# Optimization experiments

Hardware: AMD Instinct MI355X
Metric: run time of the kernel (lower is better)

Reference implementation:

```python
import jax, jax.numpy as jnp
import numpy as np

N = 50000        # nodes
E = 400000       # edges
F_IN = 128       # node feature dim
NEG_SLOPE = 0.2  # PyG GATConv default


def setup_inputs() -> dict:
    key = jax.random.key(0)
    ks = jax.random.split(key, 24)
    p = lambda k, shape: (jax.random.normal(k, shape, dtype=jnp.float32) * 0.1)
    return {
        "x": jax.random.normal(ks[0], (N, F_IN), dtype=jnp.float32),
        "edge_index": jax.random.randint(ks[1], (2, E), 0, N, dtype=jnp.int32),
        "edge_attr": jax.random.normal(ks[2], (E, 1), dtype=jnp.float32),
        "year": jax.random.normal(ks[3], (E, 1), dtype=jnp.float32),
        "quarter": jax.random.normal(ks[4], (E, 1), dtype=jnp.float32),
        "W1": p(ks[5], (4 * 128, F_IN)), "a1s": p(ks[6], (4, 128)), "a1d": p(ks[7], (4, 128)), "b1": jnp.zeros((512,), jnp.float32),
        "W2": p(ks[8], (4 * 32, 512)), "a2s": p(ks[9], (4, 32)), "a2d": p(ks[10], (4, 32)), "b2": jnp.zeros((128,), jnp.float32),
        "W3": p(ks[11], (1 * 8, 128)), "a3s": p(ks[12], (1, 8)), "a3d": p(ks[13], (1, 8)), "b3": jnp.zeros((8,), jnp.float32),
        # fc1: 8*2 + 1 + 2 = 19 -> 16 ; fc2: 16 -> 1
        "fc1_w": p(ks[14], (16, 19)), "fc1_b": jnp.zeros((16,), jnp.float32),
        "fc2_w": p(ks[15], (1, 16)), "fc2_b": jnp.zeros((1,), jnp.float32),
    }


def gat_conv(x, src, dst, W, a_s, a_d, b):
    """PyG GATConv (concat=True, self-loops already in src/dst, no dropout)."""
    H, C = a_s.shape
    n = x.shape[0]
    h = (x @ W.T).reshape(n, H, C)                      # [N,H,C]
    s = jnp.einsum("nhc,hc->nh", h, a_s)                # alpha_src per node
    d = jnp.einsum("nhc,hc->nh", h, a_d)                # alpha_dst per node
    e = jax.nn.leaky_relu(s[src] + d[dst], NEG_SLOPE)   # [E',H]
    m = jax.ops.segment_max(e, dst, num_segments=n)     # segment softmax over dst
    ex = jnp.exp(e - m[dst])
    den = jax.ops.segment_sum(ex, dst, num_segments=n)
    alpha = ex / den[dst]                               # [E',H]
    out = jax.ops.segment_sum(alpha[:, :, None] * h[src], dst, num_segments=n)
    return out.reshape(n, H * C) + b


def reference(x, edge_index, edge_attr, year, quarter,
              W1, a1s, a1d, b1, W2, a2s, a2d, b2, W3, a3s, a3d, b3,
              fc1_w, fc1_b, fc2_w, fc2_b):
    n = x.shape[0]
    loops = jnp.arange(n, dtype=edge_index.dtype)       # add_self_loops=True
    src = jnp.concatenate([edge_index[0], loops])
    dst = jnp.concatenate([edge_index[1], loops])
    h = jax.nn.elu(gat_conv(x, src, dst, W1, a1s, a1d, b1))
    h = jax.nn.elu(gat_conv(h, src, dst, W2, a2s, a2d, b2))
    h = jax.nn.elu(gat_conv(h, src, dst, W3, a3s, a3d, b3))
    z = jnp.concatenate([h[edge_index[0]], h[edge_index[1]], edge_attr, year, quarter], axis=1)
    z = jax.nn.relu(z @ fc1_w.T + fc1_b)
    return (z @ fc2_w.T + fc2_b).squeeze(-1)            # [E]
```

## Files before the change

kernel.cpp:

```cpp
#include <hip/hip_runtime.h>
#include <hip/hip_bf16.h>

#define NN 50000
#define EE 400000
#define EP 450000

typedef __attribute__((ext_vector_type(8))) short short8;
typedef __attribute__((ext_vector_type(4))) float f32x4;

__device__ __forceinline__ float us2f(unsigned short u) {
    unsigned int x = ((unsigned int)u) << 16;
    union { unsigned int i; float f; } c; c.i = x; return c.f;
}
__device__ __forceinline__ unsigned short f2bfu(float f) {
    union { float f; unsigned int u; } c; c.f = f;
    unsigned int r = c.u + 0x7FFFu + ((c.u >> 16) & 1u);
    return (unsigned short)(r >> 16);
}
__device__ __forceinline__ unsigned int pack2bf(float lo, float hi) {
    return (unsigned int)f2bfu(lo) | ((unsigned int)f2bfu(hi) << 16);
}
__device__ __forceinline__ float lrelu_exp(float x) {
    x = x > 0.f ? x : 0.2f * x;
    return __expf(x);
}


#define DEGB 1758
#define CVTB 512
__global__ void prep_kernel(const int* __restrict__ ei, int* __restrict__ deg,
                            const float* __restrict__ W1, const float* __restrict__ W2,
                            __hip_bfloat16* __restrict__ pw1, __hip_bfloat16* __restrict__ pw2,
                            const float* __restrict__ a1s, const float* __restrict__ a1d,
                            float* __restrict__ usd) {
    int b = blockIdx.x;
    if (b < DEGB) {
        int e = b * 256 + threadIdx.x;
        if (e >= EP) return;
        int dst = (e < EE) ? ei[EE + e] : e - EE;
        atomicAdd(&deg[dst], 1);
    } else if (b < DEGB + CVTB) {
        int i = (b - DEGB) * 256 + threadIdx.x;
        if (i < 65536) {
            int n = i >> 7, k = i & 127;
            int idx = ((n >> 4) * 4 + (k >> 5)) * 512 + ((k & 31) >> 3) * 128 + (n & 15) * 8 + (k & 7);
            pw1[idx] = __float2bfloat16(W1[i]);
        } else {
            int j = i - 65536;
            int n = j >> 9, k = j & 511;
            int idx = ((n >> 4) * 16 + (k >> 5)) * 512 + ((k & 31) >> 3) * 128 + (n & 15) * 8 + (k & 7);
            pw2[idx] = __float2bfloat16(W2[j]);
        }
    } else {
        int t = (b - DEGB - CVTB) * 256 + threadIdx.x;
        if (t >= 1024) return;
        int row = t >> 7, k = t & 127;
        int hh = row & 3;
        const float* av = (row < 4) ? (a1s + hh * 128) : (a1d + hh * 128);
        const float* wp = W1 + (size_t)(hh * 128) * 128 + k;
        float acc = 0.f;
        for (int c = 0; c < 128; c++) acc += av[c] * wp[(size_t)c * 128];
        usd[t] = acc;
    }
}

__global__ void cvtx_sd(const float* __restrict__ x, const float* __restrict__ usd,
                        __hip_bfloat16* __restrict__ xb,
                        float* __restrict__ s, float* __restrict__ d, int M) {
    __shared__ float us_s[1024];
    for (int i = threadIdx.x; i < 1024; i += 256) us_s[i] = usd[i];
    __syncthreads();
    int wave = threadIdx.x >> 6, lane = threadIdx.x & 63;
    int m0 = blockIdx.x * 64 + wave * 16;
    int r = lane & 15, quad = lane >> 4;
    int am = m0 + r; if (am >= M) am = M - 1;
    const float* xp = x + (size_t)am * 128 + quad * 8;
    float xv[32];
#pragma unroll
    for (int kk = 0; kk < 4; kk++) {
        float4 a = *(const float4*)(xp + kk * 32);
        float4 bq = *(const float4*)(xp + kk * 32 + 4);
        xv[kk*8+0]=a.x;  xv[kk*8+1]=a.y;  xv[kk*8+2]=a.z;  xv[kk*8+3]=a.w;
        xv[kk*8+4]=bq.x; xv[kk*8+5]=bq.y; xv[kk*8+6]=bq.z; xv[kk*8+7]=bq.w;
        short8 o;
        o[0]=(short)f2bfu(a.x);  o[1]=(short)f2bfu(a.y);
        o[2]=(short)f2bfu(a.z);  o[3]=(short)f2bfu(a.w);
        o[4]=(short)f2bfu(bq.x); o[5]=(short)f2bfu(bq.y);
        o[6]=(short)f2bfu(bq.z); o[7]=(short)f2bfu(bq.w);
        *(short8*)(xb + (size_t)am * 128 + quad * 8 + kk * 32) = o;
    }
    float acc[8];
#pragma unroll
    for (int o = 0; o < 8; o++) {
        const float* up = us_s + o * 128 + quad * 8;
        float a = 0.f;
#pragma unroll
        for (int kk = 0; kk < 4; kk++)
#pragma unroll
            for (int j = 0; j < 8; j++) a += xv[kk*8+j] * up[kk*32+j];
        acc[o] = a;
    }
#pragma unroll
    for (int o = 0; o < 8; o++) {
        acc[o] += __shfl_xor(acc[o], 16, 64);
        acc[o] += __shfl_xor(acc[o], 32, 64);
    }
    int m = m0 + r;
    if (quad == 0 && m < M) {
#pragma unroll
        for (int hh = 0; hh < 4; hh++) { s[m*4+hh] = acc[hh]; d[m*4+hh] = acc[4+hh]; }
    }
}

#define SCB 49
__global__ void scan1_kernel(const int* __restrict__ deg, int* __restrict__ bsum) {
    __shared__ int red[256];
    int b = blockIdx.x, t = threadIdx.x;
    int base = b * 1024 + t * 4;
    int s = 0;
    if (base + 3 < NN) { int4 v = *(const int4*)(deg + base); s = v.x + v.y + v.z + v.w; }
    else { for (int i = base; i < NN; i++) s += deg[i]; }
    red[t] = s;
    __syncthreads();
    for (int off = 128; off > 0; off >>= 1) {
        if (t < off) red[t] += red[t + off];
        __syncthreads();
    }
    if (t == 0) bsum[b] = red[0];
}

__global__ void scan2_kernel(const int* __restrict__ deg, const int* __restrict__ bsum,
                             int* __restrict__ offsets) {
    __shared__ int lsum[256];
    int b = blockIdx.x, t = threadIdx.x;
    int boff = 0;
    for (int i = 0; i < b; i++) boff += bsum[i];
    int base = b * 1024 + t * 4;
    int4 v = {0, 0, 0, 0};
    if (base + 3 < NN) v = *(const int4*)(deg + base);
    else {
        if (base < NN)     v.x = deg[base];
        if (base + 1 < NN) v.y = deg[base + 1];
        if (base + 2 < NN) v.z = deg[base + 2];
        if (base + 3 < NN) v.w = deg[base + 3];
    }
    int s = v.x + v.y + v.z + v.w;
    lsum[t] = s;
    __syncthreads();
    for (int off = 1; off < 256; off <<= 1) {
        int val = (t >= off) ? lsum[t - off] : 0;
        __syncthreads();
        lsum[t] += val;
        __syncthreads();
    }
    int ex = boff + (t ? lsum[t - 1] : 0);
    if (base < NN)     offsets[base]     = ex;
    if (base + 1 < NN) offsets[base + 1] = ex + v.x;
    if (base + 2 < NN) offsets[base + 2] = ex + v.x + v.y;
    if (base + 3 < NN) offsets[base + 3] = ex + v.x + v.y + v.z;
    if (b == SCB - 1 && t == 255) offsets[NN] = boff + lsum[255];
}

__global__ void fill_kernel(const int* __restrict__ ei, const int* __restrict__ offsets,
                            int* __restrict__ cursor,
                            const float* __restrict__ s1, const float* __restrict__ d1,
                            int* __restrict__ elist, int* __restrict__ dstlist,
                            float* __restrict__ welist) {
    int e = blockIdx.x * blockDim.x + threadIdx.x;
    if (e >= EP) return;
    int src, dst;
    if (e < EE) { src = ei[e]; dst = ei[EE + e]; } else { src = dst = e - EE; }
    int pos = atomicAdd(&cursor[dst], 1);
    int j = offsets[dst] + pos;
    elist[j] = src;
    dstlist[j] = dst;
    float4 sv = *(const float4*)(s1 + (size_t)src * 4);
    float4 dv = *(const float4*)(d1 + (size_t)dst * 4);
    float4 w;
    w.x = lrelu_exp(sv.x + dv.x);
    w.y = lrelu_exp(sv.y + dv.y);
    w.z = lrelu_exp(sv.z + dv.z);
    w.w = lrelu_exp(sv.w + dv.w);
    *(float4*)(welist + (size_t)j * 4) = w;
}

__global__ void edge_w4(const int* __restrict__ elist, const int* __restrict__ dstlist,
                        const float* __restrict__ s, const float* __restrict__ d,
                        float* __restrict__ wout) {
    int j = blockIdx.x * blockDim.x + threadIdx.x;
    if (j >= EP) return;
    int src = elist[j], dst = dstlist[j];
    float4 sv = *(const float4*)(s + (size_t)src * 4);
    float4 dv = *(const float4*)(d + (size_t)dst * 4);
    float4 w;
    w.x = lrelu_exp(sv.x + dv.x);
    w.y = lrelu_exp(sv.y + dv.y);
    w.z = lrelu_exp(sv.z + dv.z);
    w.w = lrelu_exp(sv.w + dv.w);
    *(float4*)(wout + (size_t)j * 4) = w;
}

__global__ void edge_w1(const int* __restrict__ elist, const int* __restrict__ dstlist,
                        const float* __restrict__ s, const float* __restrict__ d,
                        float* __restrict__ wout) {
    int j = blockIdx.x * blockDim.x + threadIdx.x;
    if (j >= EP) return;
    wout[j] = lrelu_exp(s[elist[j]] + d[dstlist[j]]);
}

__global__ __launch_bounds__(1024) void l1_fused(
        const int* __restrict__ elist, const int* __restrict__ offsets,
        const float* __restrict__ wl,
        const __hip_bfloat16* __restrict__ xb,
        const __hip_bfloat16* __restrict__ pW1,
        const float* __restrict__ b,
        __hip_bfloat16* __restrict__ pact) {
    __shared__ unsigned short frag[16 * 520];
    int w = threadIdx.x >> 6, lane = threadIdx.x & 63;
    int m0 = blockIdx.x * 16;
    int node = m0 + w;

    int j0 = __builtin_amdgcn_readfirstlane(offsets[node]);
    int j1 = __builtin_amdgcn_readfirstlane(offsets[node + 1]);
    float den0 = 0.f, den1 = 0.f, den2 = 0.f, den3 = 0.f;
    float a00=0.f,a01=0.f,a10=0.f,a11=0.f,a20=0.f,a21=0.f,a30=0.f,a31=0.f;
    const unsigned short* xp = (const unsigned short*)xb + lane * 2;
    int j = j0;
    for (; j + 4 <= j1; j += 4) {
        int sA = elist[j], sB = elist[j+1], sC = elist[j+2], sD = elist[j+3];
        float4 wA = *(const float4*)(wl + (size_t)j * 4);
        float4 wB = *(const float4*)(wl + (size_t)(j+1) * 4);
        float4 wC = *(const float4*)(wl + (size_t)(j+2) * 4);
        float4 wD = *(const float4*)(wl + (size_t)(j+3) * 4);
        unsigned int xA = *(const unsigned int*)(xp + (size_t)sA * 128);
        unsigned int xB = *(const unsigned int*)(xp + (size_t)sB * 128);
        unsigned int xC = *(const unsigned int*)(xp + (size_t)sC * 128);
        unsigned int xD = *(const unsigned int*)(xp + (size_t)sD * 128);
        float xA0 = us2f((unsigned short)xA), xA1 = us2f((unsigned short)(xA >> 16));
        float xB0 = us2f((unsigned short)xB), xB1 = us2f((unsigned short)(xB >> 16));
        float xC0 = us2f((unsigned short)xC), xC1 = us2f((unsigned short)(xC >> 16));
        float xD0 = us2f((unsigned short)xD), xD1 = us2f((unsigned short)(xD >> 16));
        den0 += (wA.x + wB.x) + (wC.x + wD.x);
        den1 += (wA.y + wB.y) + (wC.y + wD.y);
        den2 += (wA.z + wB.z) + (wC.z + wD.z);
        den3 += (wA.w + wB.w) + (wC.w + wD.w);
        a00 += wA.x*xA0 + wB.x*xB0 + wC.x*xC0 + wD.x*xD0;
        a01 += wA.x*xA1 + wB.x*xB1 + wC.x*xC1 + wD.x*xD1;
        a10 += wA.y*xA0 + wB.y*xB0 + wC.y*xC0 + wD.y*xD0;
        a11 += wA.y*xA1 + wB.y*xB1 + wC.y*xC1 + wD.y*xD1;
        a20 += wA.z*xA0 + wB.z*xB0 + wC.z*xC0 + wD.z*xD0;
        a21 += wA.z*xA1 + wB.z*xB1 + wC.z*xC1 + wD.z*xD1;
        a30 += wA.w*xA0 + wB.w*xB0 + wC.w*xC0 + wD.w*xD0;
        a31 += wA.w*xA1 + wB.w*xB1 + wC.w*xC1 + wD.w*xD1;
    }
    for (; j < j1; j++) {
        int sE = elist[j];
        float4 ww = *(const float4*)(wl + (size_t)j * 4);
        unsigned int xv = *(const unsigned int*)(xp + (size_t)sE * 128);
        float x0 = us2f((unsigned short)xv), x1 = us2f((unsigned short)(xv >> 16));
        den0 += ww.x; den1 += ww.y; den2 += ww.z; den3 += ww.w;
        a00 += ww.x*x0; a01 += ww.x*x1; a10 += ww.y*x0; a11 += ww.y*x1;
        a20 += ww.z*x0; a21 += ww.z*x1; a30 += ww.w*x0; a31 += ww.w*x1;
    }
    {
        int c0 = lane * 2;
        int fq = c0 >> 5;
        int sub = (c0 & 31) >> 3;
        int rowp = w ^ (sub << 2);
        float i0 = 1.f/den0, i1 = 1.f/den1, i2 = 1.f/den2, i3 = 1.f/den3;
        unsigned int* f32p = (unsigned int*)frag;
        int base = (fq * 520 + sub * 128 + rowp * 8 + (c0 & 7)) >> 1;
        f32p[base]             = pack2bf(a00*i0, a01*i0);
        f32p[base + 4 * 260]   = pack2bf(a10*i1, a11*i1);
        f32p[base + 8 * 260]   = pack2bf(a20*i2, a21*i2);
        f32p[base + 12 * 260]  = pack2bf(a30*i3, a31*i3);
    }
    __syncthreads();

    int hh = w >> 2, g = w & 3;
    int r = lane & 15, quad = lane >> 4;
    int lsub = lane >> 4, lrow = lane & 15;
    int prow = lrow ^ (lsub << 2);
    const unsigned short* fb = frag + lsub * 128 + prow * 8;
    short8 afrag[4];
#pragma unroll
    for (int kk = 0; kk < 4; kk++)
        afrag[kk] = *(const short8*)(fb + (hh * 4 + kk) * 520);
#pragma unroll
    for (int t = 0; t < 2; t++) {
        int nb = g * 32 + t * 16;
        const __hip_bfloat16* bp = pW1 + ((size_t)(hh * 8 + (nb >> 4)) * 4) * 512 + lane * 8;
        f32x4 acc = {0.f, 0.f, 0.f, 0.f};
#pragma unroll
        for (int kk = 0; kk < 4; kk++) {
            short8 bfr = *(const short8*)(bp + kk * 512);
            acc = __builtin_amdgcn_mfma_f32_16x16x32_bf16(afrag[kk], bfr, acc, 0, 0, 0);
        }
        int n0 = hh * 128 + nb;
        float bias = b[n0 + r];
        int kk2 = (n0 + r) >> 5;
        int sub2 = ((nb & 16) + r) >> 3;
        __hip_bfloat16* op = pact + ((size_t)blockIdx.x * 16 + kk2) * 512
                           + sub2 * 128 + (r & 7);
#pragma unroll
        for (int i = 0; i < 4; i++) {
            float v = acc[i] + bias;
            v = v > 0.f ? v : (__expf(v) - 1.0f);
            op[(quad * 4 + i) * 8] = __float2bfloat16(v);
        }
    }
}

__global__ void gemm_l2(const __hip_bfloat16* __restrict__ pA,
                        const __hip_bfloat16* __restrict__ pW2,
                        const float* __restrict__ as_, const float* __restrict__ ad_,
                        __hip_bfloat16* __restrict__ Cb,
                        float* __restrict__ s, float* __restrict__ d, int M) {
    int hh = threadIdx.x >> 6, lane = threadIdx.x & 63;
    int m0 = blockIdx.x * 16;
    int r = lane & 15, quad = lane >> 4;
    const __hip_bfloat16* ap  = pA + (size_t)(m0 >> 4) * 16 * 512 + lane * 8;
    const __hip_bfloat16* bp0 = pW2 + (size_t)(hh * 2) * 16 * 512 + lane * 8;
    const __hip_bfloat16* bp1 = bp0 + 16 * 512;
    f32x4 acc0 = {0.f, 0.f, 0.f, 0.f}, acc1 = {0.f, 0.f, 0.f, 0.f};
#pragma unroll
    for (int kk = 0; kk < 16; kk++) {
        short8 af = *(const short8*)(ap + kk * 512);
        short8 b0 = *(const short8*)(bp0 + kk * 512);
        short8 b1 = *(const short8*)(bp1 + kk * 512);
        acc0 = __builtin_amdgcn_mfma_f32_16x16x32_bf16(af, b0, acc0, 0, 0, 0);
        acc1 = __builtin_amdgcn_mfma_f32_16x16x32_bf16(af, b1, acc1, 0, 0, 0);
    }
    int n0 = hh * 32;
    float as0 = as_[n0 + r],      ad0 = ad_[n0 + r];
    float as1 = as_[n0 + 16 + r], ad1 = ad_[n0 + 16 + r];
    float sacc[4], dacc[4];
#pragma unroll
    for (int i = 0; i < 4; i++) {
        int m = m0 + quad * 4 + i;
        Cb[(size_t)m * 128 + n0 + r]      = __float2bfloat16(acc0[i]);
        Cb[(size_t)m * 128 + n0 + 16 + r] = __float2bfloat16(acc1[i]);
        sacc[i] = acc0[i] * as0 + acc1[i] * as1;
        dacc[i] = acc0[i] * ad0 + acc1[i] * ad1;
    }
#pragma unroll
    for (int mask = 1; mask <= 8; mask <<= 1) {
#pragma unroll
        for (int i = 0; i < 4; i++) {
            sacc[i] += __shfl_xor(sacc[i], mask, 64);
            dacc[i] += __shfl_xor(dacc[i], mask, 64);
        }
    }
    if (r == 0) {
#pragma unroll
        for (int i = 0; i < 4; i++) {
            int m = m0 + quad * 4 + i;
            s[m * 4 + hh] = sacc[i]; d[m * 4 + hh] = dacc[i];
        }
    }
}

__global__ void gather_l2_g8(const int* __restrict__ elist, const int* __restrict__ offsets,
                             const float* __restrict__ wl,
                             const __hip_bfloat16* __restrict__ h,
                             const float* __restrict__ b,
                             const float* __restrict__ W3,
                             const float* __restrict__ a3s, const float* __restrict__ a3d,
                             __hip_bfloat16* __restrict__ h3,
                             float* __restrict__ s, float* __restrict__ d) {
    int gid = blockIdx.x * blockDim.x + threadIdx.x;
    if (gid >= NN * 64) return;
    int node = gid >> 6;
    int lane = gid & 63;
    int c0 = lane * 2;
    int hh = lane >> 4;
    int j0 = __builtin_amdgcn_readfirstlane(offsets[node]);
    int j1 = __builtin_amdgcn_readfirstlane(offsets[node + 1]);
    float den = 0.f, acc0 = 0.f, acc1 = 0.f;
    const unsigned short* hp = (const unsigned short*)h + c0;
    int j = j0;
    for (; j + 4 <= j1; j += 4) {
        int sA = elist[j], sB = elist[j+1], sC = elist[j+2], sD = elist[j+3];
        float wA = wl[(size_t)j*4 + hh],     wB = wl[(size_t)(j+1)*4 + hh];
        float wC = wl[(size_t)(j+2)*4 + hh], wD = wl[(size_t)(j+3)*4 + hh];
        unsigned int vA = *(const unsigned int*)(hp + (size_t)sA * 128);
        unsigned int vB = *(const unsigned int*)(hp + (size_t)sB * 128);
        unsigned int vC = *(const unsigned int*)(hp + (size_t)sC * 128);
        unsigned int vD = *(const unsigned int*)(hp + (size_t)sD * 128);
        den += (wA + wB) + (wC + wD);
        acc0 += wA * us2f((unsigned short)vA) + wB * us2f((unsigned short)vB)
              + wC * us2f((unsigned short)vC) + wD * us2f((unsigned short)vD);
        acc1 += wA * us2f((unsigned short)(vA >> 16)) + wB * us2f((unsigned short)(vB >> 16))
              + wC * us2f((unsigned short)(vC >> 16)) + wD * us2f((unsigned short)(vD >> 16));
    }
    for (; j < j1; j++) {
        int sE = elist[j];
        float ww = wl[(size_t)j*4 + hh];
        unsigned int v = *(const unsigned int*)(hp + (size_t)sE * 128);
        den += ww;
        acc0 += ww * us2f((unsigned short)v);
        acc1 += ww * us2f((unsigned short)(v >> 16));
    }
    float inv = 1.0f / den;
    float v0 = acc0 * inv + b[c0];
    float v1 = acc1 * inv + b[c0 + 1];
    v0 = v0 > 0.f ? v0 : (__expf(v0) - 1.0f);
    v1 = v1 > 0.f ? v1 : (__expf(v1) - 1.0f);
    float part[8];
#pragma unroll
    for (int c = 0; c < 8; c++) {
        float2 wv = *(const float2*)(W3 + c * 128 + c0);
        part[c] = v0 * wv.x + v1 * wv.y;
    }
#pragma unroll
    for (int mask = 1; mask < 64; mask <<= 1) {
#pragma unroll
        for (int c = 0; c < 8; c++) part[c] += __shfl_xor(part[c], mask, 64);
    }
    if (lane < 8) h3[(size_t)node * 8 + lane] = __float2bfloat16(part[lane]);
    if (lane == 0) {
        float sv = 0.f, dv = 0.f;
#pragma unroll
        for (int c = 0; c < 8; c++) { sv += part[c] * a3s[c]; dv += part[c] * a3d[c]; }
        s[node] = sv; d[node] = dv;
    }
}

__global__ void gather_l3(const int* __restrict__ elist, const int* __restrict__ offsets,
                          const float* __restrict__ wl,
                          const __hip_bfloat16* __restrict__ h,
                          const float* __restrict__ b,
                          __hip_bfloat16* __restrict__ act) {
    int gid = blockIdx.x * blockDim.x + threadIdx.x;
    if (gid >= NN * 8) return;
    int node = gid >> 3, t = gid & 7;
    int j0 = offsets[node], j1 = offsets[node + 1];
    float den = 0.f, acc = 0.f;
    const unsigned short* hp = (const unsigned short*)h + t;
    int j = j0;
    for (; j + 4 <= j1; j += 4) {
        int sA = elist[j], sB = elist[j+1], sC = elist[j+2], sD = elist[j+3];
        float wA = wl[j], wB = wl[j+1], wC = wl[j+2], wD = wl[j+3];
        float xA = us2f(hp[(size_t)sA * 8]);
        float xB = us2f(hp[(size_t)sB * 8]);
        float xC = us2f(hp[(size_t)sC * 8]);
        float xD = us2f(hp[(size_t)sD * 8]);
        den += (wA + wB) + (wC + wD);
        acc += wA * xA + wB * xB + wC * xC + wD * xD;
    }
    for (; j < j1; j++) {
        int sE = elist[j];
        float w = wl[j];
        den += w;
        acc += w * us2f(hp[(size_t)sE * 8]);
    }
    float v = acc / den + b[t];
    v = v > 0.f ? v : (__expf(v) - 1.0f);
    act[(size_t)node * 8 + t] = __float2bfloat16(v);
}

__global__ void mlp_kernel(const int* __restrict__ ei,
                           const __hip_bfloat16* __restrict__ act3,
                           const float* __restrict__ ea,
                           const float* __restrict__ yr,
                           const float* __restrict__ qt,
                           const float* __restrict__ fc1w,
                           const float* __restrict__ fc1b,
                           const float* __restrict__ fc2w,
                           const float* __restrict__ fc2b,
                           float* __restrict__ outp) {
    __shared__ float w1[16 * 19], b1s[16], w2[16];
    for (int i = threadIdx.x; i < 16 * 19; i += blockDim.x) w1[i] = fc1w[i];
    if (threadIdx.x < 16) {
        b1s[threadIdx.x] = fc1b[threadIdx.x];
        w2[threadIdx.x] = fc2w[threadIdx.x];
    }
    __syncthreads();
    int e = blockIdx.x * blockDim.x + threadIdx.x;
    if (e >= EE) return;
    int src = ei[e], dst = ei[EE + e];
    short8 hs = *(const short8*)(act3 + (size_t)src * 8);
    short8 hd = *(const short8*)(act3 + (size_t)dst * 8);
    float z[19];
#pragma unroll
    for (int i = 0; i < 8; i++) z[i] = us2f((unsigned short)hs[i]);
#pragma unroll
    for (int i = 0; i < 8; i++) z[8 + i] = us2f((unsigned short)hd[i]);
    z[16] = ea[e]; z[17] = yr[e]; z[18] = qt[e];
    float acc2 = fc2b[0];
#pragma unroll
    for (int j = 0; j < 16; j++) {
        float a = b1s[j];
#pragma unroll
        for (int i = 0; i < 19; i++) a += z[i] * w1[j * 19 + i];
        a = a > 0.f ? a : 0.f;
        acc2 += a * w2[j];
    }
    outp[e] = acc2;
}

extern "C" void kernel_launch(void* const* d_in, const int* in_sizes, int n_in,
                              void* d_out, int out_size, void* d_ws, size_t ws_size,
                              hipStream_t stream) {
    const float* x    = (const float*)d_in[0];
    const int*   ei   = (const int*)d_in[1];
    const float* ea   = (const float*)d_in[2];
    const float* yr   = (const float*)d_in[3];
    const float* qt   = (const float*)d_in[4];
    const float* W1   = (const float*)d_in[5];
    const float* a1s  = (const float*)d_in[6];
    const float* a1d  = (const float*)d_in[7];
    const float* b1   = (const float*)d_in[8];
    const float* W2   = (const float*)d_in[9];
    const float* a2s  = (const float*)d_in[10];
    const float* a2d  = (const float*)d_in[11];
    const float* b2   = (const float*)d_in[12];
    const float* W3   = (const float*)d_in[13];
    const float* a3s  = (const float*)d_in[14];
    const float* a3d  = (const float*)d_in[15];
    const float* b3   = (const float*)d_in[16];
    const float* fc1w = (const float*)d_in[17];
    const float* fc1b = (const float*)d_in[18];
    const float* fc2w = (const float*)d_in[19];
    const float* fc2b = (const float*)d_in[20];
    float* outp = (float*)d_out;

    char* ws = (char*)d_ws;
    __hip_bfloat16* h_buf   = (__hip_bfloat16*)(ws);
    __hip_bfloat16* act_buf = (__hip_bfloat16*)(ws + 51200000);
    float* s_buf   = (float*)(ws + 102400000);
    float* d_buf   = (float*)(ws + 103200000);
    int*   deg     = (int*)  (ws + 104000000);
    int*   cursor  = (int*)  (ws + 104200000);
    int*   offsets = (int*)  (ws + 104400000);
    int*   elist   = (int*)  (ws + 104600016);
    __hip_bfloat16* pw1 = (__hip_bfloat16*)(ws + 106400016);
    __hip_bfloat16* pw2 = (__hip_bfloat16*)(ws + 106531088);
    float* usd  = (float*)(ws + 106662160);
    int*   bsum = (int*)  (ws + 106666256);
    float* welist = (float*)(ws + 106666512);
    int*   dstlist = (int*)(ws + 113866512);
    __hip_bfloat16* xb = act_buf;

    hipMemsetAsync(deg, 0, 2 * NN * sizeof(int), stream);
    prep_kernel<<<DEGB + CVTB + 4, 256, 0, stream>>>(ei, deg, W1, W2, pw1, pw2, a1s, a1d, usd);
    scan1_kernel<<<SCB, 256, 0, stream>>>(deg, bsum);
    scan2_kernel<<<SCB, 256, 0, stream>>>(deg, bsum, offsets);
    cvtx_sd<<<(NN + 63) / 64, 256, 0, stream>>>(x, usd, xb, s_buf, d_buf, NN);
    fill_kernel<<<(EP + 255) / 256, 256, 0, stream>>>(ei, offsets, cursor, s_buf, d_buf,
                                                      elist, dstlist, welist);

    l1_fused<<<NN / 16, 1024, 0, stream>>>(elist, offsets, welist, xb, pw1, b1, h_buf);

    gemm_l2<<<(NN + 15) / 16, 256, 0, stream>>>(
        h_buf, pw2, a2s, a2d, act_buf, s_buf, d_buf, NN);
    edge_w4<<<(EP + 255) / 256, 256, 0, stream>>>(elist, dstlist, s_buf, d_buf, welist);

    gather_l2_g8<<<(NN * 64 + 255) / 256, 256, 0, stream>>>(
        elist, offsets, welist, act_buf, b2, W3, a3s, a3d, h_buf, s_buf, d_buf);

    edge_w1<<<(EP + 255) / 256, 256, 0, stream>>>(elist, dstlist, s_buf, d_buf, welist);
    gather_l3<<<(NN * 8 + 255) / 256, 256, 0, stream>>>(
        elist, offsets, welist, h_buf, b3, act_buf);

    mlp_kernel<<<(EE + 255) / 256, 256, 0, stream>>>(ei, act_buf, ea, yr, qt,
                                                     fc1w, fc1b, fc2w, fc2b, outp);
}
```

Baseline: 308.4 us.

## Fuse edge-weight computation into gathers and process two nodes per wave in layer 1

Removes the edge_w4 and edge_w1 kernels and the dstlist buffer. Layers 2 and 3 now compute the leaky-relu and exp attention weights inline in the gather loops from per-node s/d scores, with separate s3/d3 buffers so layer-3 scores no longer overwrite the layer-2 ones being read. This saves two launches and the edge-weight write/read traffic, at the cost of redundant exp work per lane and an extra random gather of s2. The layer-1 fused kernel drops to 512 threads, each wave aggregating two destination nodes with interleaved loops and four MFMA column tiles instead of two.

```diff
diff --git a/kernel.cpp b/kernel.cpp
--- a/kernel.cpp
+++ b/kernel.cpp
@@ -164,8 +164,7 @@
 __global__ void fill_kernel(const int* __restrict__ ei, const int* __restrict__ offsets,
                             int* __restrict__ cursor,
                             const float* __restrict__ s1, const float* __restrict__ d1,
-                            int* __restrict__ elist, int* __restrict__ dstlist,
-                            float* __restrict__ welist) {
+                            int* __restrict__ elist, float* __restrict__ welist) {
     int e = blockIdx.x * blockDim.x + threadIdx.x;
     if (e >= EP) return;
     int src, dst;
@@ -173,7 +172,6 @@
     int pos = atomicAdd(&cursor[dst], 1);
     int j = offsets[dst] + pos;
     elist[j] = src;
-    dstlist[j] = dst;
     float4 sv = *(const float4*)(s1 + (size_t)src * 4);
     float4 dv = *(const float4*)(d1 + (size_t)dst * 4);
     float4 w;
@@ -184,31 +182,17 @@
     *(float4*)(welist + (size_t)j * 4) = w;
 }
 
-__global__ void edge_w4(const int* __restrict__ elist, const int* __restrict__ dstlist,
-                        const float* __restrict__ s, const float* __restrict__ d,
-                        float* __restrict__ wout) {
-    int j = blockIdx.x * blockDim.x + threadIdx.x;
-    if (j >= EP) return;
-    int src = elist[j], dst = dstlist[j];
-    float4 sv = *(const float4*)(s + (size_t)src * 4);
-    float4 dv = *(const float4*)(d + (size_t)dst * 4);
-    float4 w;
-    w.x = lrelu_exp(sv.x + dv.x);
-    w.y = lrelu_exp(sv.y + dv.y);
-    w.z = lrelu_exp(sv.z + dv.z);
-    w.w = lrelu_exp(sv.w + dv.w);
-    *(float4*)(wout + (size_t)j * 4) = w;
-}
-
-__global__ void edge_w1(const int* __restrict__ elist, const int* __restrict__ dstlist,
-                        const float* __restrict__ s, const float* __restrict__ d,
-                        float* __restrict__ wout) {
-    int j = blockIdx.x * blockDim.x + threadIdx.x;
-    if (j >= EP) return;
-    wout[j] = lrelu_exp(s[elist[j]] + d[dstlist[j]]);
-}
-
-__global__ __launch_bounds__(1024) void l1_fused(
+__device__ __forceinline__ void acc_edge(float (&den)[4], float (&acc)[8],
+                                         float4 w, unsigned int x) {
+    float x0 = us2f((unsigned short)x), x1 = us2f((unsigned short)(x >> 16));
+    den[0] += w.x; den[1] += w.y; den[2] += w.z; den[3] += w.w;
+    acc[0] += w.x * x0; acc[1] += w.x * x1;
+    acc[2] += w.y * x0; acc[3] += w.y * x1;
+    acc[4] += w.z * x0; acc[5] += w.z * x1;
+    acc[6] += w.w * x0; acc[7] += w.w * x1;
+}
+
+__global__ void l1_fused(
         const int* __restrict__ elist, const int* __restrict__ offsets,
         const float* __restrict__ wl,
         const __hip_bfloat16* __restrict__ xb,
@@ -218,66 +202,87 @@
     __shared__ unsigned short frag[16 * 520];
     int w = threadIdx.x >> 6, lane = threadIdx.x & 63;
     int m0 = blockIdx.x * 16;
-    int node = m0 + w;
-
-    int j0 = __builtin_amdgcn_readfirstlane(offsets[node]);
-    int j1 = __builtin_amdgcn_readfirstlane(offsets[node + 1]);
-    float den0 = 0.f, den1 = 0.f, den2 = 0.f, den3 = 0.f;
-    float a00=0.f,a01=0.f,a10=0.f,a11=0.f,a20=0.f,a21=0.f,a30=0.f,a31=0.f;
+    int nA = m0 + 2 * w;
+
+    int ja  = __builtin_amdgcn_readfirstlane(offsets[nA]);
+    int jA1 = __builtin_amdgcn_readfirstlane(offsets[nA + 1]);
+    int jB1 = __builtin_amdgcn_readfirstlane(offsets[nA + 2]);
+    int jb = jA1;
+
+    float dA[4] = {0.f,0.f,0.f,0.f}, dB[4] = {0.f,0.f,0.f,0.f};
+    float aA[8] = {0.f,0.f,0.f,0.f,0.f,0.f,0.f,0.f};
+    float aB[8] = {0.f,0.f,0.f,0.f,0.f,0.f,0.f,0.f};
     const unsigned short* xp = (const unsigned short*)xb + lane * 2;
-    int j = j0;
-    for (; j + 4 <= j1; j += 4) {
-        int sA = elist[j], sB = elist[j+1], sC = elist[j+2], sD = elist[j+3];
-        float4 wA = *(const float4*)(wl + (size_t)j * 4);
-        float4 wB = *(const float4*)(wl + (size_t)(j+1) * 4);
-        float4 wC = *(const float4*)(wl + (size_t)(j+2) * 4);
-        float4 wD = *(const float4*)(wl + (size_t)(j+3) * 4);
-        unsigned int xA = *(const unsigned int*)(xp + (size_t)sA * 128);
-        unsigned int xB = *(const unsigned int*)(xp + (size_t)sB * 128);
-        unsigned int xC = *(const unsigned int*)(xp + (size_t)sC * 128);
-        unsigned int xD = *(const unsigned int*)(xp + (size_t)sD * 128);
-        float xA0 = us2f((unsigned short)xA), xA1 = us2f((unsigned short)(xA >> 16));
-        float xB0 = us2f((unsigned short)xB), xB1 = us2f((unsigned short)(xB >> 16));
-        float xC0 = us2f((unsigned short)xC), xC1 = us2f((unsigned short)(xC >> 16));
-        float xD0 = us2f((unsigned short)xD), xD1 = us2f((unsigned short)(xD >> 16));
-        den0 += (wA.x + wB.x) + (wC.x + wD.x);
-        den1 += (wA.y + wB.y) + (wC.y + wD.y);
-        den2 += (wA.z + wB.z) + (wC.z + wD.z);
-        den3 += (wA.w + wB.w) + (wC.w + wD.w);
-        a00 += wA.x*xA0 + wB.x*xB0 + wC.x*xC0 + wD.x*xD0;
-        a01 += wA.x*xA1 + wB.x*xB1 + wC.x*xC1 + wD.x*xD1;
-        a10 += wA.y*xA0 + wB.y*xB0 + wC.y*xC0 + wD.y*xD0;
-        a11 += wA.y*xA1 + wB.y*xB1 + wC.y*xC1 + wD.y*xD1;
-        a20 += wA.z*xA0 + wB.z*xB0 + wC.z*xC0 + wD.z*xD0;
-        a21 += wA.z*xA1 + wB.z*xB1 + wC.z*xC1 + wD.z*xD1;
-        a30 += wA.w*xA0 + wB.w*xB0 + wC.w*xC0 + wD.w*xD0;
-        a31 += wA.w*xA1 + wB.w*xB1 + wC.w*xC1 + wD.w*xD1;
-    }
-    for (; j < j1; j++) {
-        int sE = elist[j];
-        float4 ww = *(const float4*)(wl + (size_t)j * 4);
-        unsigned int xv = *(const unsigned int*)(xp + (size_t)sE * 128);
-        float x0 = us2f((unsigned short)xv), x1 = us2f((unsigned short)(xv >> 16));
-        den0 += ww.x; den1 += ww.y; den2 += ww.z; den3 += ww.w;
-        a00 += ww.x*x0; a01 += ww.x*x1; a10 += ww.y*x0; a11 += ww.y*x1;
-        a20 += ww.z*x0; a21 += ww.z*x1; a30 += ww.w*x0; a31 += ww.w*x1;
-    }
+    const float4* wl4 = (const float4*)wl;
+
+    while (ja + 2 <= jA1 && jb + 2 <= jB1) {
+        int s0 = elist[ja], s1 = elist[ja + 1];
+        int s2 = elist[jb], s3 = elist[jb + 1];
+        float4 w0 = wl4[ja], w1 = wl4[ja + 1];
+        float4 w2 = wl4[jb], w3 = wl4[jb + 1];
+        unsigned int x0 = *(const unsigned int*)(xp + (size_t)s0 * 128);
+        unsigned int x1 = *(const unsigned int*)(xp + (size_t)s1 * 128);
+        unsigned int x2 = *(const unsigned int*)(xp + (size_t)s2 * 128);
+        unsigned int x3 = *(const unsigned int*)(xp + (size_t)s3 * 128);
+        acc_edge(dA, aA, w0, x0); acc_edge(dA, aA, w1, x1);
+        acc_edge(dB, aB, w2, x2); acc_edge(dB, aB, w3, x3);
+        ja += 2; jb += 2;
+    }
+    while (ja + 2 <= jA1) {
+        int s0 = elist[ja], s1 = elist[ja + 1];
+        float4 w0 = wl4[ja], w1 = wl4[ja + 1];
+        unsigned int x0 = *(const unsigned int*)(xp + (size_t)s0 * 128);
+        unsigned int x1 = *(const unsigned int*)(xp + (size_t)s1 * 128);
+        acc_edge(dA, aA, w0, x0); acc_edge(dA, aA, w1, x1);
+        ja += 2;
+    }
+    while (jb + 2 <= jB1) {
+        int s0 = elist[jb], s1 = elist[jb + 1];
+        float4 w0 = wl4[jb], w1 = wl4[jb + 1];
+        unsigned int x0 = *(const unsigned int*)(xp + (size_t)s0 * 128);
+        unsigned int x1 = *(const unsigned int*)(xp + (size_t)s1 * 128);
+        acc_edge(dB, aB, w0, x0); acc_edge(dB, aB, w1, x1);
+        jb += 2;
+    }
+    if (ja < jA1) {
+        int s0 = elist[ja]; float4 w0 = wl4[ja];
+        unsigned int x0 = *(const unsigned int*)(xp + (size_t)s0 * 128);
+        acc_edge(dA, aA, w0, x0);
+    }
+    if (jb < jB1) {
+        int s0 = elist[jb]; float4 w0 = wl4[jb];
+        unsigned int x0 = *(const unsigned int*)(xp + (size_t)s0 * 128);
+        acc_edge(dB, aB, w0, x0);
+    }
+
     {
         int c0 = lane * 2;
         int fq = c0 >> 5;
         int sub = (c0 & 31) >> 3;
-        int rowp = w ^ (sub << 2);
-        float i0 = 1.f/den0, i1 = 1.f/den1, i2 = 1.f/den2, i3 = 1.f/den3;
         unsigned int* f32p = (unsigned int*)frag;
-        int base = (fq * 520 + sub * 128 + rowp * 8 + (c0 & 7)) >> 1;
-        f32p[base]             = pack2bf(a00*i0, a01*i0);
-        f32p[base + 4 * 260]   = pack2bf(a10*i1, a11*i1);
-        f32p[base + 8 * 260]   = pack2bf(a20*i2, a21*i2);
-        f32p[base + 12 * 260]  = pack2bf(a30*i3, a31*i3);
+        int base0 = fq * 260 + sub * 64 + (c0 & 7) / 2;
+        {
+            int rowp = (2 * w) ^ (sub << 2);
+            int base = base0 + rowp * 4;
+            float i0 = 1.f/dA[0], i1 = 1.f/dA[1], i2 = 1.f/dA[2], i3 = 1.f/dA[3];
+            f32p[base]            = pack2bf(aA[0]*i0, aA[1]*i0);
+            f32p[base + 4 * 260]  = pack2bf(aA[2]*i1, aA[3]*i1);
+            f32p[base + 8 * 260]  = pack2bf(aA[4]*i2, aA[5]*i2);
+            f32p[base + 12 * 260] = pack2bf(aA[6]*i3, aA[7]*i3);
+        }
+        {
+            int rowp = (2 * w + 1) ^ (sub << 2);
+            int base = base0 + rowp * 4;
+            float i0 = 1.f/dB[0], i1 = 1.f/dB[1], i2 = 1.f/dB[2], i3 = 1.f/dB[3];
+            f32p[base]            = pack2bf(aB[0]*i0, aB[1]*i0);
+            f32p[base + 4 * 260]  = pack2bf(aB[2]*i1, aB[3]*i1);
+            f32p[base + 8 * 260]  = pack2bf(aB[4]*i2, aB[5]*i2);
+            f32p[base + 12 * 260] = pack2bf(aB[6]*i3, aB[7]*i3);
+        }
     }
     __syncthreads();
 
-    int hh = w >> 2, g = w & 3;
+    int hh = w >> 1, half = w & 1;
     int r = lane & 15, quad = lane >> 4;
     int lsub = lane >> 4, lrow = lane & 15;
     int prow = lrow ^ (lsub << 2);
@@ -287,8 +292,8 @@
     for (int kk = 0; kk < 4; kk++)
         afrag[kk] = *(const short8*)(fb + (hh * 4 + kk) * 520);
 #pragma unroll
-    for (int t = 0; t < 2; t++) {
-        int nb = g * 32 + t * 16;
+    for (int t = 0; t < 4; t++) {
+        int nb = half * 64 + t * 16;
         const __hip_bfloat16* bp = pW1 + ((size_t)(hh * 8 + (nb >> 4)) * 4) * 512 + lane * 8;
         f32x4 acc = {0.f, 0.f, 0.f, 0.f};
 #pragma unroll
@@ -361,13 +366,13 @@
 }
 
 __global__ void gather_l2_g8(const int* __restrict__ elist, const int* __restrict__ offsets,
-                             const float* __restrict__ wl,
+                             const float* __restrict__ s2, const float* __restrict__ d2,
                              const __hip_bfloat16* __restrict__ h,
                              const float* __restrict__ b,
                              const float* __restrict__ W3,
                              const float* __restrict__ a3s, const float* __restrict__ a3d,
                              __hip_bfloat16* __restrict__ h3,
-                             float* __restrict__ s, float* __restrict__ d) {
+                             float* __restrict__ s3, float* __restrict__ d3) {
     int gid = blockIdx.x * blockDim.x + threadIdx.x;
     if (gid >= NN * 64) return;
     int node = gid >> 6;
@@ -376,17 +381,20 @@
     int hh = lane >> 4;
     int j0 = __builtin_amdgcn_readfirstlane(offsets[node]);
     int j1 = __builtin_amdgcn_readfirstlane(offsets[node + 1]);
+    float dv = d2[node * 4 + hh];
     float den = 0.f, acc0 = 0.f, acc1 = 0.f;
     const unsigned short* hp = (const unsigned short*)h + c0;
     int j = j0;
     for (; j + 4 <= j1; j += 4) {
         int sA = elist[j], sB = elist[j+1], sC = elist[j+2], sD = elist[j+3];
-        float wA = wl[(size_t)j*4 + hh],     wB = wl[(size_t)(j+1)*4 + hh];
-        float wC = wl[(size_t)(j+2)*4 + hh], wD = wl[(size_t)(j+3)*4 + hh];
+        float eA = s2[sA * 4 + hh] + dv, eB = s2[sB * 4 + hh] + dv;
+        float eC = s2[sC * 4 + hh] + dv, eD = s2[sD * 4 + hh] + dv;
         unsigned int vA = *(const unsigned int*)(hp + (size_t)sA * 128);
         unsigned int vB = *(const unsigned int*)(hp + (size_t)sB * 128);
         unsigned int vC = *(const unsigned int*)(hp + (size_t)sC * 128);
         unsigned int vD = *(const unsigned int*)(hp + (size_t)sD * 128);
+        float wA = lrelu_exp(eA), wB = lrelu_exp(eB);
+        float wC = lrelu_exp(eC), wD = lrelu_exp(eD);
         den += (wA + wB) + (wC + wD);
         acc0 += wA * us2f((unsigned short)vA) + wB * us2f((unsigned short)vB)
               + wC * us2f((unsigned short)vC) + wD * us2f((unsigned short)vD);
@@ -395,7 +403,7 @@
     }
     for (; j < j1; j++) {
         int sE = elist[j];
-        float ww = wl[(size_t)j*4 + hh];
+        float ww = lrelu_exp(s2[sE * 4 + hh] + dv);
         unsigned int v = *(const unsigned int*)(hp + (size_t)sE * 128);
         den += ww;
         acc0 += ww * us2f((unsigned short)v);
@@ -419,15 +427,15 @@
     }
     if (lane < 8) h3[(size_t)node * 8 + lane] = __float2bfloat16(part[lane]);
     if (lane == 0) {
-        float sv = 0.f, dv = 0.f;
-#pragma unroll
-        for (int c = 0; c < 8; c++) { sv += part[c] * a3s[c]; dv += part[c] * a3d[c]; }
-        s[node] = sv; d[node] = dv;
+        float sv = 0.f, dvv = 0.f;
+#pragma unroll
+        for (int c = 0; c < 8; c++) { sv += part[c] * a3s[c]; dvv += part[c] * a3d[c]; }
+        s3[node] = sv; d3[node] = dvv;
     }
 }
 
 __global__ void gather_l3(const int* __restrict__ elist, const int* __restrict__ offsets,
-                          const float* __restrict__ wl,
+                          const float* __restrict__ s3, const float* __restrict__ d3,
                           const __hip_bfloat16* __restrict__ h,
                           const float* __restrict__ b,
                           __hip_bfloat16* __restrict__ act) {
@@ -435,12 +443,14 @@
     if (gid >= NN * 8) return;
     int node = gid >> 3, t = gid & 7;
     int j0 = offsets[node], j1 = offsets[node + 1];
+    float dnode = d3[node];
     float den = 0.f, acc = 0.f;
     const unsigned short* hp = (const unsigned short*)h + t;
     int j = j0;
     for (; j + 4 <= j1; j += 4) {
         int sA = elist[j], sB = elist[j+1], sC = elist[j+2], sD = elist[j+3];
-        float wA = wl[j], wB = wl[j+1], wC = wl[j+2], wD = wl[j+3];
+        float wA = lrelu_exp(s3[sA] + dnode), wB = lrelu_exp(s3[sB] + dnode);
+        float wC = lrelu_exp(s3[sC] + dnode), wD = lrelu_exp(s3[sD] + dnode);
         float xA = us2f(hp[(size_t)sA * 8]);
         float xB = us2f(hp[(size_t)sB * 8]);
         float xC = us2f(hp[(size_t)sC * 8]);
@@ -450,7 +460,7 @@
     }
     for (; j < j1; j++) {
         int sE = elist[j];
-        float w = wl[j];
+        float w = lrelu_exp(s3[sE] + dnode);
         den += w;
         acc += w * us2f(hp[(size_t)sE * 8]);
     }
@@ -539,7 +549,8 @@
     float* usd  = (float*)(ws + 106662160);
     int*   bsum = (int*)  (ws + 106666256);
     float* welist = (float*)(ws + 106666512);
-    int*   dstlist = (int*)(ws + 113866512);
+    float* s3_buf = (float*)(ws + 113866512);
+    float* d3_buf = (float*)(ws + 114071312);
     __hip_bfloat16* xb = act_buf;
 
     hipMemsetAsync(deg, 0, 2 * NN * sizeof(int), stream);
@@ -548,20 +559,19 @@
     scan2_kernel<<<SCB, 256, 0, stream>>>(deg, bsum, offsets);
     cvtx_sd<<<(NN + 63) / 64, 256, 0, stream>>>(x, usd, xb, s_buf, d_buf, NN);
     fill_kernel<<<(EP + 255) / 256, 256, 0, stream>>>(ei, offsets, cursor, s_buf, d_buf,
-                                                      elist, dstlist, welist);
-
-    l1_fused<<<NN / 16, 1024, 0, stream>>>(elist, offsets, welist, xb, pw1, b1, h_buf);
+                                                      elist, welist);
+
+    l1_fused<<<NN / 16, 512, 0, stream>>>(elist, offsets, welist, xb, pw1, b1, h_buf);
 
     gemm_l2<<<(NN + 15) / 16, 256, 0, stream>>>(
         h_buf, pw2, a2s, a2d, act_buf, s_buf, d_buf, NN);
-    edge_w4<<<(EP + 255) / 256, 256, 0, stream>>>(elist, dstlist, s_buf, d_buf, welist);
 
     gather_l2_g8<<<(NN * 64 + 255) / 256, 256, 0, stream>>>(
-        elist, offsets, welist, act_buf, b2, W3, a3s, a3d, h_buf, s_buf, d_buf);
-
-    edge_w1<<<(EP + 255) / 256, 256, 0, stream>>>(elist, dstlist, s_buf, d_buf, welist);
+        elist, offsets, s_buf, d_buf, act_buf, b2, W3, a3s, a3d,
+        h_buf, s3_buf, d3_buf);
+
     gather_l3<<<(NN * 8 + 255) / 256, 256, 0, stream>>>(
-        elist, offsets, welist, h_buf, b3, act_buf);
+        elist, offsets, s3_buf, d3_buf, h_buf, b3, act_buf);
 
     mlp_kernel<<<(EE + 255) / 256, 256, 0, stream>>>(ei, act_buf, ea, yr, qt,
                                                      fc1w, fc1b, fc2w, fc2b, outp);
```

After: 298.8 us. -3.1%, faster.
